# Performance work log

Measured on AMD Instinct MI355X. Metric: run time of the kernel, lower is better.

The kernel has to match this reference:

```python
import jax, jax.numpy as jnp
import numpy as np

BETA = 0.99      # rootfind_module beta
TOL = 1e-3       # torch loop: while V(fx*a) - t > 0.001
MAX_ITER = 50    # safety cap (torch loop is uncapped but converges)


def _fhat(x, W1, b1, W2, b2):
    # x: (B,1,D) -> (B,1,D)
    h = jnp.tanh(x @ W1 + b1)
    return h @ W2 + b2


def _V_sample(z, Wv1, Wv2):
    # z: (1,D) -> scalar Lyapunov value
    h = jnp.tanh(z @ Wv1)
    y = h @ Wv2
    return jnp.sum(y * y) + 0.01 * jnp.sum(z * z)


def _V(z, Wv1, Wv2):
    # z: (B,1,D) -> (B,1,1)
    h = jnp.tanh(z @ Wv1)
    y = h @ Wv2
    v = jnp.sum(y * y, axis=(-2, -1)) + 0.01 * jnp.sum(z * z, axis=(-2, -1))
    return v[:, None, None]


def _newton_step(fhatx, target, alpha, Wv1, Wv2):
    # newton_iter.forward: F = alpha - (V(fhatx*alpha) - target) / dV/dalpha
    z = fhatx * alpha                                  # (B,1,D)
    Vz = _V(z, Wv1, Wv2)                               # (B,1,1)
    gradV = jax.vmap(jax.grad(_V_sample), in_axes=(0, None, None))(z, Wv1, Wv2)
    dV_da = jnp.sum(gradV * fhatx, axis=(-2, -1))[:, None, None]
    return alpha - (Vz - target) / dV_da


def _rootfind(fhatx, target, Wv1, Wv2):
    # batched, masked replacement of torch per-sample Python while loops
    B = fhatx.shape[0]
    alpha0 = jnp.ones((B, 1, 1), fhatx.dtype)

    def cond(carry):
        i, alpha = carry
        resid = _V(fhatx * alpha, Wv1, Wv2) - target
        return jnp.logical_and(i < MAX_ITER, jnp.any(resid > TOL))

    def body(carry):
        i, alpha = carry
        resid = _V(fhatx * alpha, Wv1, Wv2) - target
        new_alpha = _newton_step(fhatx, target, alpha, Wv1, Wv2)
        alpha = jnp.where(resid > TOL, new_alpha, alpha)  # only unconverged samples move
        return (i + 1, alpha)

    _, alpha = jax.lax.while_loop(cond, body, (jnp.int32(0), alpha0))
    return alpha


def setup_inputs() -> dict:
    key = jax.random.key(0)
    ks = jax.random.split(key, 5)
    B, D, H, HV, VO = 8192, 512, 2048, 512, 256
    s = 0.02
    return {
        "x": jax.random.normal(ks[0], (B, 1, D), jnp.float32),
        "W1": jax.random.normal(ks[1], (D, H), jnp.float32) * s,
        "b1": jnp.zeros((H,), jnp.float32),
        "W2": jax.random.normal(ks[2], (H, D), jnp.float32) * s,
        "b2": jnp.zeros((D,), jnp.float32),
        "Wv1": jax.random.normal(ks[3], (D, HV), jnp.float32) * s,
        "Wv2": jax.random.normal(ks[4], (HV, VO), jnp.float32) * s,
    }


def reference(x, W1, b1, W2, b2, Wv1, Wv2):
    fhatx = _fhat(x, W1, b1, W2, b2)        # (B,1,D)
    target = BETA * _V(x, Wv1, Wv2)         # (B,1,1)
    alpha = _rootfind(fhatx, target, Wv1, Wv2)
    return fhatx * alpha                    # x_root, (B,1,D)
```

## Files before the change

### kernel.cpp

```cpp
#include <hip/hip_runtime.h>
#include <hip/hip_bf16.h>
#include <stdint.h>
#include <stddef.h>

typedef __bf16 bf16_t;
typedef __bf16 bf16x8 __attribute__((ext_vector_type(8)));
typedef __bf16 bf16x4 __attribute__((ext_vector_type(4)));
typedef float  f32x4  __attribute__((ext_vector_type(4)));

#define NB 8192
#define ND 512
#define NH 2048
#define NHV 512
#define NVO 256
#define RF_TOL 1e-3f
#define NEWTON_MAX 16

typedef const __attribute__((address_space(1))) void gvoid_t;
typedef __attribute__((address_space(3))) void lvoid_t;

__device__ __forceinline__ void gload_lds16(const void* g, void* l) {
  __builtin_amdgcn_global_load_lds((gvoid_t*)g, (lvoid_t*)l, 16, 0, 0);
}

__device__ __forceinline__ float fast_tanhf(float x) {
  x = fminf(fmaxf(x, -15.0f), 15.0f);
  float e = __expf(2.0f * x);
  return (e - 1.0f) * __builtin_amdgcn_rcpf(e + 1.0f);
}

struct GJob {
  const bf16_t* A;
  const bf16_t* Bt;
  const float*  bias;
  bf16_t* Cbf;
  float*  Cf;
  int N, K, nbx, tanh_act;
};

template<int BM>
__global__ __launch_bounds__(256, 4)
void gemm_kernel(GJob j0, GJob j1)
{
  constexpr int MI = BM / 32;
  __shared__ bf16_t As[BM * 64];
  __shared__ bf16_t Bs[128 * 64];
  const bool first = (int)blockIdx.x < j0.nbx;
  const GJob jb = first ? j0 : j1;
  const int bx = (int)blockIdx.x - (first ? 0 : j0.nbx);
  const int K = jb.K, N = jb.N;

  const int t = threadIdx.x, lane = t & 63, w = t >> 6;
  const int wm = w >> 1, wn = w & 1;
  const int la = lane & 15, lg = lane >> 4;
  const size_t m0 = (size_t)blockIdx.y * BM, n0 = (size_t)bx * 128;

  size_t soffA[MI], soffB[4]; int doff[4];
#pragma unroll
  for (int j = 0; j < 4; ++j) {
    const int off = t * 16 + j * 4096;
    const int r = off >> 7, c = off & 127;
    const size_t so = (size_t)r * K + ((c ^ ((r & 7) << 4)) >> 1);
    if (j < MI) soffA[j] = so;
    soffB[j] = so;
    doff[j] = off;
  }
  const bf16_t* Ab = jb.A + m0 * K;
  const bf16_t* Bb = jb.Bt + n0 * K;

  int abyte[MI][2], bbyte[4][2];
#pragma unroll
  for (int ks = 0; ks < 2; ++ks) {
#pragma unroll
    for (int i = 0; i < MI; ++i) {
      const int ra = wm * (BM / 2) + i * 16 + la;
      abyte[i][ks] = ra * 128 + ((ks * 64 + lg * 16) ^ ((ra & 7) << 4));
    }
#pragma unroll
    for (int j = 0; j < 4; ++j) {
      const int rb = wn * 64 + j * 16 + la;
      bbyte[j][ks] = rb * 128 + ((ks * 64 + lg * 16) ^ ((rb & 7) << 4));
    }
  }

  f32x4 acc[MI][4] = {};
  const int nsteps = K >> 6;

  for (int ts = 0; ts < nsteps; ++ts) {
    const int k0 = ts << 6;
#pragma unroll
    for (int j = 0; j < MI; ++j)
      gload_lds16(Ab + soffA[j] + k0, (char*)As + doff[j]);
#pragma unroll
    for (int j = 0; j < 4; ++j)
      gload_lds16(Bb + soffB[j] + k0, (char*)Bs + doff[j]);
    __syncthreads();

    bf16x8 afr[MI][2], bfr[4][2];
#pragma unroll
    for (int ks = 0; ks < 2; ++ks) {
#pragma unroll
      for (int i = 0; i < MI; ++i)
        afr[i][ks] = *(const bf16x8*)((const char*)As + abyte[i][ks]);
#pragma unroll
      for (int j = 0; j < 4; ++j)
        bfr[j][ks] = *(const bf16x8*)((const char*)Bs + bbyte[j][ks]);
    }
#pragma unroll
    for (int ks = 0; ks < 2; ++ks)
#pragma unroll
      for (int i = 0; i < MI; ++i)
#pragma unroll
        for (int j = 0; j < 4; ++j)
          acc[i][j] = __builtin_amdgcn_mfma_f32_16x16x32_bf16(afr[i][ks], bfr[j][ks], acc[i][j], 0, 0, 0);
    __syncthreads();
  }

#pragma unroll
  for (int i = 0; i < MI; ++i) {
#pragma unroll
    for (int j = 0; j < 4; ++j) {
      const size_t col = n0 + wn * 64 + j * 16 + la;
      const float bv = jb.bias ? jb.bias[col] : 0.0f;
#pragma unroll
      for (int r = 0; r < 4; ++r) {
        const size_t row = m0 + wm * (BM / 2) + i * 16 + lg * 4 + r;
        float v = acc[i][j][r] + bv;
        if (jb.tanh_act) v = fast_tanhf(v);
        if (jb.Cbf) jb.Cbf[row * N + col] = (bf16_t)v;
        if (jb.Cf)  jb.Cf [row * N + col] = v;
      }
    }
  }
}

__device__ __forceinline__ void tr_body(const float* __restrict__ src, bf16_t* __restrict__ dst,
                                        int R, int C, int bidx, float (*tile)[33]) {
  const int tilesx = C >> 5;
  const int bi = (bidx / tilesx) << 5, bj = (bidx % tilesx) << 5;
  const int t = threadIdx.x, tx = t & 31, ty = t >> 5;
#pragma unroll
  for (int r = ty; r < 32; r += 8)
    tile[r][tx] = src[(size_t)(bi + r) * C + (bj + tx)];
  __syncthreads();
#pragma unroll
  for (int r = ty; r < 32; r += 8)
    dst[(size_t)(bj + r) * R + (bi + tx)] = (bf16_t)tile[tx][r];
}

__global__ void prep_kernel(const float* __restrict__ x, bf16_t* __restrict__ xbf, float* __restrict__ xsq,
                            const float* __restrict__ W1, bf16_t* __restrict__ w1t,
                            const float* __restrict__ W2, bf16_t* __restrict__ w2t,
                            const float* __restrict__ Wv1, bf16_t* __restrict__ wv1t,
                            const float* __restrict__ Wv2, bf16_t* __restrict__ wv2t)
{
  __shared__ float tile[32][33];
  const int b = blockIdx.x;
  if (b < 1024)      tr_body(W1, w1t, 512, 2048, b, tile);
  else if (b < 2048) tr_body(W2, w2t, 2048, 512, b - 1024, tile);
  else if (b < 2304) tr_body(Wv1, wv1t, 512, 512, b - 2048, tile);
  else if (b < 2432) tr_body(Wv2, wv2t, 512, 256, b - 2304, tile);
  else {
    const int t = threadIdx.x;
    const int row = (b - 2432) * 4 + (t >> 6), l = t & 63;
    const float4* sr = (const float4*)(x + (size_t)row * ND);
    bf16x4* dw = (bf16x4*)(xbf + (size_t)row * ND);
    float s = 0.0f;
#pragma unroll
    for (int c = l; c < ND / 4; c += 64) {
      float4 v = sr[c];
      s = fmaf(v.x, v.x, fmaf(v.y, v.y, fmaf(v.z, v.z, fmaf(v.w, v.w, s))));
      bf16x4 o;
      o[0] = (bf16_t)v.x; o[1] = (bf16_t)v.y; o[2] = (bf16_t)v.z; o[3] = (bf16_t)v.w;
      dw[c] = o;
    }
#pragma unroll
    for (int m = 32; m; m >>= 1) s += __shfl_xor(s, m);
    if (l == 0) xsq[row] = s;
  }
}

__global__ void post_kernel(const bf16_t* __restrict__ fbf, const float* __restrict__ yx,
                            const float* __restrict__ xsq,
                            float* __restrict__ fsq, float* __restrict__ tgt)
{
  const int b = blockIdx.x, t = threadIdx.x, l = t & 63;
  if (t < 64) {
    bf16x8 v = *(const bf16x8*)(fbf + (size_t)b * ND + l * 8);
    float s = 0.0f;
#pragma unroll
    for (int q = 0; q < 8; ++q) { float f = (float)v[q]; s = fmaf(f, f, s); }
#pragma unroll
    for (int m = 32; m; m >>= 1) s += __shfl_xor(s, m);
    if (l == 0) fsq[b] = s;
  } else {
    float4 v = ((const float4*)(yx + (size_t)b * NVO))[l];
    float s = fmaf(v.x, v.x, fmaf(v.y, v.y, fmaf(v.z, v.z, v.w * v.w)));
#pragma unroll
    for (int m = 32; m; m >>= 1) s += __shfl_xor(s, m);
    if (l == 0) tgt[b] = 0.99f * (s + 0.01f * xsq[b]);
  }
}

__global__ __launch_bounds__(512, 2)
void newton_kernel(const bf16_t* __restrict__ u0, const bf16_t* __restrict__ Wv2t,
                   const float* __restrict__ fsq, const float* __restrict__ tgt,
                   const float* __restrict__ fhat, float* __restrict__ out)
{
  __shared__ alignas(16) bf16_t hs[32 * 512];
  __shared__ alignas(16) bf16_t es[32 * 512];
  __shared__ float red[8][32][2];
  __shared__ float alpha_s[32], fsq_s[32], tgt_s[32];
  __shared__ int notdone_s;

  const int t = threadIdx.x, lane = t & 63, w = t >> 6;
  const int la = lane & 15, lg = lane >> 4;
  const int s_base = blockIdx.x * 32;
  const int arow = lane & 31, ahi = lane >> 5;

  bf16x8 bfr[2][16];
#pragma unroll
  for (int nt = 0; nt < 2; ++nt) {
    const bf16_t* bp = Wv2t + (size_t)(w * 32 + nt * 16 + la) * NHV + lg * 8;
#pragma unroll
    for (int k = 0; k < 16; ++k)
      bfr[nt][k] = *(const bf16x8*)(bp + k * 32);
  }

  bf16x8 ureg[4];
#pragma unroll
  for (int i = 0; i < 4; ++i)
    ureg[i] = *(const bf16x8*)(u0 + (size_t)(s_base + arow) * NHV + (w * 8 + ahi * 4 + i) * 8);

  if (t < 32) {
    alpha_s[t] = 1.0f;
    fsq_s[t] = fsq[s_base + t];
    tgt_s[t] = tgt[s_base + t];
  }
  __syncthreads();

  for (int it = 0; it < NEWTON_MAX; ++it) {
    {
      const float c2 = 2.0f * alpha_s[arow];
#pragma unroll
      for (int i = 0; i < 4; ++i) {
        const int k8 = w * 8 + ahi * 4 + i;
        const int byte = (arow << 10) + ((k8 ^ (arow & 7)) << 4);
        bf16x8 uv = ureg[i], hf, ef;
#pragma unroll
        for (int q = 0; q < 8; ++q) {
          float u = (float)uv[q];
          float e = __expf(c2 * u);
          float h = (e - 1.0f) * __builtin_amdgcn_rcpf(e + 1.0f);
          hf[q] = (bf16_t)h;
          ef[q] = (bf16_t)(u * (1.0f - h * h));
        }
        *(bf16x8*)((char*)hs + byte) = hf;
        *(bf16x8*)((char*)es + byte) = ef;
      }
    }
    __syncthreads();

    f32x4 accy[2][2] = {};
    f32x4 accw[2][2] = {};
#pragma unroll
    for (int k = 0; k < 16; ++k) {
#pragma unroll
      for (int mt = 0; mt < 2; ++mt) {
        const int row = mt * 16 + la;
        const int byte = (row << 10) + (((k * 4 + lg) ^ (row & 7)) << 4);
        bf16x8 hf = *(const bf16x8*)((const char*)hs + byte);
        bf16x8 ef = *(const bf16x8*)((const char*)es + byte);
#pragma unroll
        for (int nt = 0; nt < 2; ++nt) {
          accy[mt][nt] = __builtin_amdgcn_mfma_f32_16x16x32_bf16(hf, bfr[nt][k], accy[mt][nt], 0, 0, 0);
          accw[mt][nt] = __builtin_amdgcn_mfma_f32_16x16x32_bf16(ef, bfr[nt][k], accw[mt][nt], 0, 0, 0);
        }
      }
    }

#pragma unroll
    for (int mt = 0; mt < 2; ++mt) {
#pragma unroll
      for (int r = 0; r < 4; ++r) {
        float sy = 0.0f, sw = 0.0f;
#pragma unroll
        for (int nt = 0; nt < 2; ++nt) {
          float yv = accy[mt][nt][r], wv = accw[mt][nt][r];
          sy = fmaf(yv, yv, sy);
          sw = fmaf(yv, wv, sw);
        }
        sy += __shfl_xor(sy, 1); sw += __shfl_xor(sw, 1);
        sy += __shfl_xor(sy, 2); sw += __shfl_xor(sw, 2);
        sy += __shfl_xor(sy, 4); sw += __shfl_xor(sw, 4);
        sy += __shfl_xor(sy, 8); sw += __shfl_xor(sw, 8);
        if (la == 0) {
          red[w][mt * 16 + lg * 4 + r][0] = sy;
          red[w][mt * 16 + lg * 4 + r][1] = sw;
        }
      }
    }
    __syncthreads();
    if (t < 32) {
      float SY = 0.0f, SW = 0.0f;
#pragma unroll
      for (int w8 = 0; w8 < 8; ++w8) {
        SY += red[w8][t][0];
        SW += red[w8][t][1];
      }
      float a = alpha_s[t];
      const float fs = fsq_s[t];
      const float V = SY + 0.01f * a * a * fs;
      const float dV = 2.0f * SW + 0.02f * a * fs;
      const float resid = V - tgt_s[t];
      const bool go = resid > RF_TOL;
      if (go) alpha_s[t] = a - resid / dV;
      const int nd = __any(go);
      if (t == 0) notdone_s = nd;
    }
    __syncthreads();
    if (!notdone_s) break;
  }

  {
    const int r = t >> 4;
    const int c4 = t & 15;
    const float a = alpha_s[r];
    const size_t rb = (size_t)(s_base + r) * ND;
    const float4* sp = (const float4*)(fhat + rb);
    float4* dp = (float4*)(out + rb);
#pragma unroll
    for (int jj = 0; jj < 8; ++jj) {
      float4 v = sp[c4 + jj * 16];
      v.x *= a; v.y *= a; v.z *= a; v.w *= a;
      dp[c4 + jj * 16] = v;
    }
  }
}

extern "C" void kernel_launch(void* const* d_in, const int* in_sizes, int n_in,
                              void* d_out, int out_size, void* d_ws, size_t ws_size,
                              hipStream_t stream)
{
  (void)in_sizes; (void)n_in; (void)out_size; (void)ws_size;
  const float* x   = (const float*)d_in[0];
  const float* W1  = (const float*)d_in[1];
  const float* b1  = (const float*)d_in[2];
  const float* W2  = (const float*)d_in[3];
  const float* b2  = (const float*)d_in[4];
  const float* Wv1 = (const float*)d_in[5];
  const float* Wv2 = (const float*)d_in[6];
  float* out = (float*)d_out;

  char* ws = (char*)d_ws;
  size_t off = 0;
  auto alloc = [&](size_t n) { char* p = ws + off; off += (n + 255) & ~(size_t)255; return p; };

  bf16_t* xbf  = (bf16_t*)alloc((size_t)NB * ND * 2);
  bf16_t* w1t  = (bf16_t*)alloc((size_t)NH * ND * 2);
  bf16_t* w2t  = (bf16_t*)alloc((size_t)ND * NH * 2);
  bf16_t* wv1t = (bf16_t*)alloc((size_t)NHV * ND * 2);
  bf16_t* wv2t = (bf16_t*)alloc((size_t)NVO * NHV * 2);
  bf16_t* h1   = (bf16_t*)alloc((size_t)NB * NH * 2);
  float*  fhat = (float*)alloc((size_t)NB * ND * 4);
  bf16_t* fbf  = (bf16_t*)alloc((size_t)NB * ND * 2);
  bf16_t* hx   = (bf16_t*)alloc((size_t)NB * NHV * 2);
  float*  yx   = (float*)alloc((size_t)NB * NVO * 4);
  bf16_t* u0bf = (bf16_t*)alloc((size_t)NB * NHV * 2);
  float*  xsq  = (float*)alloc((size_t)NB * 4);
  float*  fsq  = (float*)alloc((size_t)NB * 4);
  float*  tgt  = (float*)alloc((size_t)NB * 4);

  prep_kernel<<<4480, 256, 0, stream>>>(x, xbf, xsq, W1, w1t, W2, w2t, Wv1, wv1t, Wv2, wv2t);

  GJob jh1 { xbf, w1t,  b1,      h1,  nullptr, NH,  ND, NH  / 128, 1 };
  GJob jhx { xbf, wv1t, nullptr, hx,  nullptr, NHV, ND, NHV / 128, 1 };
  gemm_kernel<128><<<dim3(NH / 128 + NHV / 128, NB / 128), 256, 0, stream>>>(jh1, jhx);

  GJob jf  { h1,  w2t,  b2,      fbf, fhat,    ND,  NH, ND  / 128, 0 };
  GJob jy  { hx,  wv2t, nullptr, nullptr, yx,  NVO, NHV, NVO / 128, 0 };
  gemm_kernel<64><<<dim3(ND / 128 + NVO / 128, NB / 64), 256, 0, stream>>>(jf, jy);

  post_kernel<<<NB, 128, 0, stream>>>(fbf, yx, xsq, fsq, tgt);

  GJob ju  { fbf, wv1t, nullptr, u0bf, nullptr, NHV, ND, NHV / 128, 0 };
  gemm_kernel<64><<<dim3(NHV / 128, NB / 64), 256, 0, stream>>>(ju, ju);

  newton_kernel<<<NB / 32, 512, 0, stream>>>(u0bf, wv2t, fsq, tgt, fhat, out);
}
```

Measured before the change: 125.1 us.

## Add 256x256-tile double-buffered GEMM for first layer with XCD-aware block remap

Adds a new GEMM kernel with 256x256 output tiles, 512 threads and a double-buffered LDS prefetch pipeline. The block index is remapped across the 8 XCDs. It replaces the 128x128 kernel for the fused x@W1 / x@Wv1 tanh GEMM. The aim is more operand reuse per tile and overlap of global loads with MFMA work. In exchange it uses 128KB of LDS and a large accumulator register footprint, and it launches only 320 blocks, which may limit occupancy and wave balance.

```diff
diff --git a/kernel.cpp b/kernel.cpp
--- a/kernel.cpp
+++ b/kernel.cpp
@@ -37,6 +37,115 @@
   float*  Cf;
   int N, K, nbx, tanh_act;
 };
+
+__global__ __launch_bounds__(512, 2)
+void gemm256_kernel(GJob j0, GJob j1)
+{
+  __shared__ bf16_t As[2 * 256 * 64];
+  __shared__ bf16_t Bs[2 * 256 * 64];
+
+  int f = (int)blockIdx.y * (int)gridDim.x + (int)blockIdx.x;
+  const int nwg = (int)gridDim.x * (int)gridDim.y;
+  f = (f & 7) * (nwg >> 3) + (f >> 3);
+  const int bx0 = f % (int)gridDim.x, by = f / (int)gridDim.x;
+
+  const bool first = bx0 < j0.nbx;
+  const GJob jb = first ? j0 : j1;
+  const int bx = bx0 - (first ? 0 : j0.nbx);
+  const int K = jb.K, N = jb.N;
+
+  const int t = threadIdx.x, lane = t & 63, w = t >> 6;
+  const int wm = w >> 2, wn = w & 3;
+  const int la = lane & 15, lg = lane >> 4;
+  const size_t m0 = (size_t)by * 256, n0 = (size_t)bx * 256;
+
+  int soff[4];
+#pragma unroll
+  for (int j = 0; j < 4; ++j) {
+    const int off = t * 16 + j * 8192;
+    const int r = off >> 7, c = off & 127;
+    soff[j] = r * K + ((c ^ ((r & 7) << 4)) >> 1);
+  }
+  const bf16_t* Ab = jb.A + m0 * K;
+  const bf16_t* Bb = jb.Bt + n0 * K;
+
+  const int swz = (la & 7) << 4;
+  const int sw0 = (lg * 16) ^ swz;
+  const int sw1 = (64 + lg * 16) ^ swz;
+  const int abase = (wm * 128 + la) * 128;
+  const int bbase = (wn * 64 + la) * 128;
+
+  f32x4 acc[8][4] = {};
+  const int NT = K >> 6;
+
+#pragma unroll
+  for (int j = 0; j < 4; ++j) gload_lds16(Ab + soff[j], (char*)As + (t * 16 + j * 8192));
+#pragma unroll
+  for (int j = 0; j < 4; ++j) gload_lds16(Bb + soff[j], (char*)Bs + (t * 16 + j * 8192));
+#pragma unroll
+  for (int j = 0; j < 4; ++j) gload_lds16(Ab + soff[j] + 64, (char*)As + 32768 + (t * 16 + j * 8192));
+#pragma unroll
+  for (int j = 0; j < 4; ++j) gload_lds16(Bb + soff[j] + 64, (char*)Bs + 32768 + (t * 16 + j * 8192));
+
+  for (int ts = 0; ts < NT; ++ts) {
+    if (ts < NT - 1) asm volatile("s_waitcnt vmcnt(8)" ::: "memory");
+    else             asm volatile("s_waitcnt vmcnt(0)" ::: "memory");
+    __builtin_amdgcn_s_barrier();
+    asm volatile("" ::: "memory");
+
+    const char* pa = (const char*)As + (ts & 1) * 32768;
+    const char* pb = (const char*)Bs + (ts & 1) * 32768;
+    bf16x8 afr[8][2], bfr[4][2];
+#pragma unroll
+    for (int i = 0; i < 8; ++i) {
+      afr[i][0] = *(const bf16x8*)(pa + abase + i * 2048 + sw0);
+      afr[i][1] = *(const bf16x8*)(pa + abase + i * 2048 + sw1);
+    }
+#pragma unroll
+    for (int j = 0; j < 4; ++j) {
+      bfr[j][0] = *(const bf16x8*)(pb + bbase + j * 2048 + sw0);
+      bfr[j][1] = *(const bf16x8*)(pb + bbase + j * 2048 + sw1);
+    }
+    asm volatile("s_waitcnt lgkmcnt(0)" ::: "memory");
+    __builtin_amdgcn_s_barrier();
+    asm volatile("" ::: "memory");
+
+    if (ts + 2 < NT) {
+      const int k0 = (ts + 2) << 6;
+      char* da = (char*)As + (ts & 1) * 32768;
+      char* db = (char*)Bs + (ts & 1) * 32768;
+#pragma unroll
+      for (int j = 0; j < 4; ++j) gload_lds16(Ab + soff[j] + k0, da + (t * 16 + j * 8192));
+#pragma unroll
+      for (int j = 0; j < 4; ++j) gload_lds16(Bb + soff[j] + k0, db + (t * 16 + j * 8192));
+    }
+
+#pragma unroll
+    for (int ks = 0; ks < 2; ++ks)
+#pragma unroll
+      for (int i = 0; i < 8; ++i)
+#pragma unroll
+        for (int j = 0; j < 4; ++j)
+          acc[i][j] = __builtin_amdgcn_mfma_f32_16x16x32_bf16(afr[i][ks], bfr[j][ks], acc[i][j], 0, 0, 0);
+  }
+
+#pragma unroll
+  for (int i = 0; i < 8; ++i) {
+#pragma unroll
+    for (int j = 0; j < 4; ++j) {
+      const size_t col = n0 + wn * 64 + j * 16 + la;
+      const float bv = jb.bias ? jb.bias[col] : 0.0f;
+#pragma unroll
+      for (int r = 0; r < 4; ++r) {
+        const size_t row = m0 + wm * 128 + i * 16 + lg * 4 + r;
+        float v = acc[i][j][r] + bv;
+        if (jb.tanh_act) v = fast_tanhf(v);
+        if (jb.Cbf) jb.Cbf[row * N + col] = (bf16_t)v;
+        if (jb.Cf)  jb.Cf [row * N + col] = v;
+      }
+    }
+  }
+}
 
 template<int BM>
 __global__ __launch_bounds__(256, 4)
@@ -373,9 +482,9 @@
 
   prep_kernel<<<4480, 256, 0, stream>>>(x, xbf, xsq, W1, w1t, W2, w2t, Wv1, wv1t, Wv2, wv2t);
 
-  GJob jh1 { xbf, w1t,  b1,      h1,  nullptr, NH,  ND, NH  / 128, 1 };
-  GJob jhx { xbf, wv1t, nullptr, hx,  nullptr, NHV, ND, NHV / 128, 1 };
-  gemm_kernel<128><<<dim3(NH / 128 + NHV / 128, NB / 128), 256, 0, stream>>>(jh1, jhx);
+  GJob jh1 { xbf, w1t,  b1,      h1,  nullptr, NH,  ND, NH  / 256, 1 };
+  GJob jhx { xbf, wv1t, nullptr, hx,  nullptr, NHV, ND, NHV / 256, 1 };
+  gemm256_kernel<<<dim3(NH / 256 + NHV / 256, NB / 256), 512, 0, stream>>>(jh1, jhx);
 
   GJob jf  { h1,  w2t,  b2,      fbf, fhat,    ND,  NH, ND  / 128, 0 };
   GJob jy  { hx,  wv2t, nullptr, nullptr, yx,  NVO, NHV, NVO / 128, 0 };
```

Result: slower. 137.2 us (+9.6%).

## Fuse post reductions and u0 GEMM into the Newton kernel

Applied to the files above, without the earlier changes.

The separate post_kernel (squared-norm and target reductions) and the fbf×Wv1 GEMM producing u0 are folded into the Newton kernel's prologue. Each block loads its 32 fhat rows into LDS, computes fsq and target locally, and runs a small MFMA GEMM against Wv1 from global memory to build u in LDS. This removes two launches and the u0/fsq/tgt round trips through global memory. In exchange every block rereads all of Wv1 from global or L2, and launch bounds drop to one block per CU, which may lower occupancy.

```diff
diff --git a/kernel.cpp b/kernel.cpp
--- a/kernel.cpp
+++ b/kernel.cpp
@@ -180,31 +180,10 @@
   }
 }
 
-__global__ void post_kernel(const bf16_t* __restrict__ fbf, const float* __restrict__ yx,
-                            const float* __restrict__ xsq,
-                            float* __restrict__ fsq, float* __restrict__ tgt)
-{
-  const int b = blockIdx.x, t = threadIdx.x, l = t & 63;
-  if (t < 64) {
-    bf16x8 v = *(const bf16x8*)(fbf + (size_t)b * ND + l * 8);
-    float s = 0.0f;
-#pragma unroll
-    for (int q = 0; q < 8; ++q) { float f = (float)v[q]; s = fmaf(f, f, s); }
-#pragma unroll
-    for (int m = 32; m; m >>= 1) s += __shfl_xor(s, m);
-    if (l == 0) fsq[b] = s;
-  } else {
-    float4 v = ((const float4*)(yx + (size_t)b * NVO))[l];
-    float s = fmaf(v.x, v.x, fmaf(v.y, v.y, fmaf(v.z, v.z, v.w * v.w)));
-#pragma unroll
-    for (int m = 32; m; m >>= 1) s += __shfl_xor(s, m);
-    if (l == 0) tgt[b] = 0.99f * (s + 0.01f * xsq[b]);
-  }
-}
-
-__global__ __launch_bounds__(512, 2)
-void newton_kernel(const bf16_t* __restrict__ u0, const bf16_t* __restrict__ Wv2t,
-                   const float* __restrict__ fsq, const float* __restrict__ tgt,
+__global__ __launch_bounds__(512, 1)
+void newton_kernel(const bf16_t* __restrict__ fbf, const bf16_t* __restrict__ wv1t,
+                   const bf16_t* __restrict__ Wv2t,
+                   const float* __restrict__ yx, const float* __restrict__ xsq,
                    const float* __restrict__ fhat, float* __restrict__ out)
 {
   __shared__ alignas(16) bf16_t hs[32 * 512];
@@ -218,6 +197,73 @@
   const int s_base = blockIdx.x * 32;
   const int arow = lane & 31, ahi = lane >> 5;
 
+  {
+    const int row = t >> 4, c0 = (t & 15) * 4;
+    float s = 0.0f;
+#pragma unroll
+    for (int i = 0; i < 4; ++i) {
+      const int k8 = c0 + i;
+      bf16x8 v = *(const bf16x8*)(fbf + (size_t)(s_base + row) * ND + k8 * 8);
+#pragma unroll
+      for (int q = 0; q < 8; ++q) { float f = (float)v[q]; s = fmaf(f, f, s); }
+      *(bf16x8*)((char*)hs + (row << 10) + ((k8 ^ (row & 7)) << 4)) = v;
+    }
+    s += __shfl_xor(s, 1); s += __shfl_xor(s, 2); s += __shfl_xor(s, 4); s += __shfl_xor(s, 8);
+    if ((t & 15) == 0) fsq_s[row] = s;
+  }
+  {
+    const int smp = t >> 4;
+    const float4* yp = (const float4*)(yx + (size_t)(s_base + smp) * NVO + (t & 15) * 16);
+    float s = 0.0f;
+#pragma unroll
+    for (int i = 0; i < 4; ++i) {
+      float4 v = yp[i];
+      s = fmaf(v.x, v.x, fmaf(v.y, v.y, fmaf(v.z, v.z, fmaf(v.w, v.w, s))));
+    }
+    s += __shfl_xor(s, 1); s += __shfl_xor(s, 2); s += __shfl_xor(s, 4); s += __shfl_xor(s, 8);
+    if ((t & 15) == 0) tgt_s[smp] = 0.99f * (s + 0.01f * xsq[s_base + smp]);
+  }
+  if (t < 32) alpha_s[t] = 1.0f;
+  __syncthreads();
+
+  f32x4 uacc[2][4] = {};
+#pragma unroll
+  for (int k = 0; k < 16; ++k) {
+    bf16x8 afr[2];
+#pragma unroll
+    for (int mt = 0; mt < 2; ++mt) {
+      const int row = mt * 16 + la;
+      afr[mt] = *(const bf16x8*)((const char*)hs + (row << 10) + (((k * 4 + lg) ^ (row & 7)) << 4));
+    }
+#pragma unroll
+    for (int nt = 0; nt < 4; ++nt) {
+      const bf16x8 b = *(const bf16x8*)(wv1t + (size_t)(w * 64 + nt * 16 + la) * ND + k * 32 + lg * 8);
+#pragma unroll
+      for (int mt = 0; mt < 2; ++mt)
+        uacc[mt][nt] = __builtin_amdgcn_mfma_f32_16x16x32_bf16(afr[mt], b, uacc[mt][nt], 0, 0, 0);
+    }
+  }
+
+#pragma unroll
+  for (int mt = 0; mt < 2; ++mt)
+#pragma unroll
+    for (int nt = 0; nt < 4; ++nt)
+#pragma unroll
+      for (int r = 0; r < 4; ++r) {
+        const int row = mt * 16 + lg * 4 + r;
+        const int col = w * 64 + nt * 16 + la;
+        *(bf16_t*)((char*)es + (row << 10) + (((col >> 3) ^ (row & 7)) << 4) + (col & 7) * 2)
+            = (bf16_t)uacc[mt][nt][r];
+      }
+  __syncthreads();
+
+  bf16x8 ureg[4];
+#pragma unroll
+  for (int i = 0; i < 4; ++i) {
+    const int k8 = w * 8 + ahi * 4 + i;
+    ureg[i] = *(const bf16x8*)((const char*)es + (arow << 10) + ((k8 ^ (arow & 7)) << 4));
+  }
+
   bf16x8 bfr[2][16];
 #pragma unroll
   for (int nt = 0; nt < 2; ++nt) {
@@ -225,17 +271,6 @@
 #pragma unroll
     for (int k = 0; k < 16; ++k)
       bfr[nt][k] = *(const bf16x8*)(bp + k * 32);
-  }
-
-  bf16x8 ureg[4];
-#pragma unroll
-  for (int i = 0; i < 4; ++i)
-    ureg[i] = *(const bf16x8*)(u0 + (size_t)(s_base + arow) * NHV + (w * 8 + ahi * 4 + i) * 8);
-
-  if (t < 32) {
-    alpha_s[t] = 1.0f;
-    fsq_s[t] = fsq[s_base + t];
-    tgt_s[t] = tgt[s_base + t];
   }
   __syncthreads();
 
@@ -366,10 +401,7 @@
   bf16_t* fbf  = (bf16_t*)alloc((size_t)NB * ND * 2);
   bf16_t* hx   = (bf16_t*)alloc((size_t)NB * NHV * 2);
   float*  yx   = (float*)alloc((size_t)NB * NVO * 4);
-  bf16_t* u0bf = (bf16_t*)alloc((size_t)NB * NHV * 2);
   float*  xsq  = (float*)alloc((size_t)NB * 4);
-  float*  fsq  = (float*)alloc((size_t)NB * 4);
-  float*  tgt  = (float*)alloc((size_t)NB * 4);
 
   prep_kernel<<<4480, 256, 0, stream>>>(x, xbf, xsq, W1, w1t, W2, w2t, Wv1, wv1t, Wv2, wv2t);
 
@@ -381,10 +413,5 @@
   GJob jy  { hx,  wv2t, nullptr, nullptr, yx,  NVO, NHV, NVO / 128, 0 };
   gemm_kernel<64><<<dim3(ND / 128 + NVO / 128, NB / 64), 256, 0, stream>>>(jf, jy);
 
-  post_kernel<<<NB, 128, 0, stream>>>(fbf, yx, xsq, fsq, tgt);
-
-  GJob ju  { fbf, wv1t, nullptr, u0bf, nullptr, NHV, ND, NHV / 128, 0 };
-  gemm_kernel<64><<<dim3(NHV / 128, NB / 64), 256, 0, stream>>>(ju, ju);
-
-  newton_kernel<<<NB / 32, 512, 0, stream>>>(u0bf, wv2t, fsq, tgt, fhat, out);
-}
+  newton_kernel<<<NB / 32, 512, 0, stream>>>(fbf, wv1t, wv2t, yx, xsq, fhat, out);
+}
```

Result: no change. 124.7 us (-0.4%).
